# Kernel optimization log

Hardware: AMD Instinct MI355X
Metric: run time of the kernel (lower is better)

The kernel has to match this reference:

```python
import jax, jax.numpy as jnp
from jax import lax
import numpy as np

# dims
N_DIA, DLEN = 48, 64            # 48 dialogues, 64 utterances each
N = N_DIA * DLEN                # total utterances = 3072
D = 512                         # n_dim (modal feature dim)
H = 512                         # nhidden
NL = 2                          # GCNII layers
NS = 2                          # n_speakers
ALPHA, LAMDA = 0.1, 0.5
PI = float(np.pi)
SCALE = 0.99999                 # acos clamp factor from original code


def setup_inputs() -> dict:
    key = jax.random.key(0)
    ks = jax.random.split(key, 8)
    a = jax.random.normal(ks[0], (N, D), jnp.float32)
    v = jax.random.normal(ks[1], (N, D), jnp.float32)
    l = jax.random.normal(ks[2], (N, D), jnp.float32)
    qmask = jax.random.uniform(ks[3], (DLEN, N_DIA, NS), jnp.float32)
    dia_len = np.full((N_DIA,), DLEN, dtype=np.int64)  # static segment lengths
    # learned params
    W_spk = 0.02 * jax.random.normal(ks[4], (NS, D), jnp.float32)      # speaker_embeddings
    W0 = jax.random.normal(ks[5], (D, H), jnp.float32) / np.sqrt(D)    # graph_net.fcs[0]
    b0 = jnp.zeros((H,), jnp.float32)
    Wg = jax.random.normal(ks[6], (NL, H, H), jnp.float32) / np.sqrt(H)  # GCNII conv weights
    return {"a": a, "v": v, "l": l, "qmask": qmask, "dia_len": dia_len,
            "W_spk": W_spk, "W0": W0, "b0": b0, "Wg": Wg}


def _angular_sim(cs):
    # 1 - acos(cs*0.99999)/pi, clipped for numerical safety of acos
    return 1.0 - jnp.arccos(jnp.clip(cs * SCALE, -SCALE, SCALE)) / PI


def _build_adj(feats, seg_mask):
    # feats: list of 3 arrays [N, D]; seg_mask: [N, N] same-dialogue block mask
    n = feats[0].shape[0]
    normed = [f * jax.lax.rsqrt(jnp.sum(f * f, axis=1, keepdims=True)) for f in feats]
    adj = jnp.zeros((3 * n, 3 * n), feats[0].dtype)
    ar = jnp.arange(n)
    for m in range(3):
        for nn_ in range(3):
            if m == nn_:
                # within-modality: block-diagonal (per dialogue) angular cosine similarity
                sim = _angular_sim(normed[m] @ normed[m].T) * seg_mask
                adj = adj.at[m * n:(m + 1) * n, nn_ * n:(nn_ + 1) * n].set(sim)
            else:
                # cross-modality: only diagonal (same utterance) entries
                cs = jnp.sum(normed[m] * normed[nn_], axis=1)
                adj = adj.at[m * n + ar, nn_ * n + ar].set(_angular_sim(cs))
    # symmetric degree normalization D^-1/2 A D^-1/2
    dinv = jax.lax.rsqrt(adj.sum(axis=1))
    return adj * dinv[:, None] * dinv[None, :]


def reference(a, v, l, qmask, dia_len, W_spk, W0, b0, Wg):
    dl = np.asarray(dia_len)
    nb = dl.shape[0]
    # node -> (position-in-dialogue, dialogue-id), static from dia_len
    dia_id = np.repeat(np.arange(nb), dl)
    pos = np.concatenate([np.arange(x) for x in dl])
    qflat = qmask[pos, dia_id]                 # [N, NS], matches torch.cat order
    spk_idx = jnp.argmax(qflat, axis=-1)       # [N]
    l = l + W_spk[spk_idx]                     # use_speaker=True, 'l' in modals

    seg = jnp.asarray(dia_id)
    seg_mask = (seg[:, None] == seg[None, :]).astype(a.dtype)  # [N, N]
    adj = _build_adj([a, v, l], seg_mask)      # [3N, 3N]

    x = jnp.concatenate([a, v, l], axis=0)     # [3N, D]
    # GCNII_lyc (eval mode: dropout is identity)
    h0 = jax.nn.relu(x @ W0 + b0)              # [3N, H]
    thetas = jnp.log(LAMDA / jnp.arange(1, NL + 1, dtype=x.dtype) + 1.0)

    def step(h, wt):
        W, theta = wt
        hi = adj @ h
        support = (1.0 - ALPHA) * hi + ALPHA * h0   # variant=False
        h = jax.nn.relu(theta * (support @ W) + (1.0 - theta) * support)
        return h, None

    h, _ = lax.scan(step, h0, (Wg, thetas))
    feat = jnp.concatenate([x, h], axis=-1)    # use_residue=True -> [3N, D+H]
    n = a.shape[0]
    # regroup per-utterance modal features: [N, 3*(D+H)]
    out = jnp.concatenate([feat[:n], feat[n:2 * n], feat[2 * n:3 * n]], axis=-1)
    return out
```

## Files before the change

kernel.cpp:

```cpp
#include <hip/hip_runtime.h>
#include <math.h>

#define N_DIA 48
#define NTOT  3072
#define DD    512
#define M3    9216
#define SEG   ((size_t)NTOT * DD)

#define SCALE_F 0.99999f
#define PI_F    3.14159274101257324f

typedef __attribute__((ext_vector_type(8))) short frag8;
typedef __attribute__((ext_vector_type(4))) float f32x4;

__device__ __forceinline__ float ang_sim(float cs) {
    float cc = cs * SCALE_F;
    cc = fminf(fmaxf(cc, -SCALE_F), SCALE_F);
    return 1.0f - acosf(cc) / PI_F;
}
__device__ __forceinline__ unsigned short f2bf(float x) {
    union { float f; unsigned int u; } c; c.f = x;
    unsigned int r = c.u + 0x7fffu + ((c.u >> 16) & 1u);
    return (unsigned short)(r >> 16);
}
__device__ __forceinline__ float bf2f(unsigned short h) {
    union { unsigned int u; float f; } c; c.u = ((unsigned int)h) << 16;
    return c.f;
}
__device__ __forceinline__ void gload16(const unsigned short* g, unsigned short* s) {
    __builtin_amdgcn_global_load_lds(
        (const __attribute__((address_space(1))) unsigned int*)g,
        (__attribute__((address_space(3))) unsigned int*)s, 16, 0, 0);
}

__global__ __launch_bounds__(256) void k_pre_wt(
    const float* __restrict__ a, const float* __restrict__ v,
    const float* __restrict__ l, const float* __restrict__ qmask,
    const float* __restrict__ Wspk, const float* __restrict__ W0,
    const float* __restrict__ Wg,
    float* __restrict__ out, unsigned short* __restrict__ xb,
    float* __restrict__ invn, float* __restrict__ cross,
    unsigned short* __restrict__ Wt)
{
    __shared__ float tile[32][33];
    int b = blockIdx.x;
    if (b < 768) {
        int wv = threadIdx.x >> 6, t = threadIdx.x & 63;
        int i = b * 4 + wv;
        int pos = i & 63, dia = i >> 6;
        int qb = (pos * N_DIA + dia) * 2;
        float q0 = qmask[qb], q1 = qmask[qb + 1];
        int spk = (q0 >= q1) ? 0 : 1;
        const float4* av4 = (const float4*)(a + (size_t)i * DD);
        const float4* vv4 = (const float4*)(v + (size_t)i * DD);
        const float4* lv4 = (const float4*)(l + (size_t)i * DD);
        const float4* wv4 = (const float4*)(Wspk + (size_t)spk * DD);
        float* ob = out + (size_t)i * 3072;
        float saa = 0, svv = 0, sll = 0, sav = 0, sal = 0, svl = 0;
#pragma unroll
        for (int e = 0; e < 2; e++) {
            int idx = t * 2 + e;
            float4 xa = av4[idx], xv = vv4[idx], xd = lv4[idx], xw = wv4[idx];
            float4 xL = make_float4(xd.x + xw.x, xd.y + xw.y, xd.z + xw.z, xd.w + xw.w);
            *(float4*)(ob + idx * 4)        = xa;
            *(float4*)(ob + 1024 + idx * 4) = xv;
            *(float4*)(ob + 2048 + idx * 4) = xL;
            ushort4 ya, yv, yl;
            ya.x = f2bf(xa.x); ya.y = f2bf(xa.y); ya.z = f2bf(xa.z); ya.w = f2bf(xa.w);
            yv.x = f2bf(xv.x); yv.y = f2bf(xv.y); yv.z = f2bf(xv.z); yv.w = f2bf(xv.w);
            yl.x = f2bf(xL.x); yl.y = f2bf(xL.y); yl.z = f2bf(xL.z); yl.w = f2bf(xL.w);
            *(ushort4*)(xb + (size_t)i * DD + idx * 4) = ya;
            *(ushort4*)(xb + SEG + (size_t)i * DD + idx * 4) = yv;
            *(ushort4*)(xb + 2 * SEG + (size_t)i * DD + idx * 4) = yl;
            saa += xa.x * xa.x + xa.y * xa.y + xa.z * xa.z + xa.w * xa.w;
            svv += xv.x * xv.x + xv.y * xv.y + xv.z * xv.z + xv.w * xv.w;
            sll += xL.x * xL.x + xL.y * xL.y + xL.z * xL.z + xL.w * xL.w;
            sav += xa.x * xv.x + xa.y * xv.y + xa.z * xv.z + xa.w * xv.w;
            sal += xa.x * xL.x + xa.y * xL.y + xa.z * xL.z + xa.w * xL.w;
            svl += xv.x * xL.x + xv.y * xL.y + xv.z * xL.z + xv.w * xL.w;
        }
#pragma unroll
        for (int off = 32; off; off >>= 1) {
            saa += __shfl_down(saa, off, 64);
            svv += __shfl_down(svv, off, 64);
            sll += __shfl_down(sll, off, 64);
            sav += __shfl_down(sav, off, 64);
            sal += __shfl_down(sal, off, 64);
            svl += __shfl_down(svl, off, 64);
        }
        if (t == 0) {
            float ina = 1.0f / sqrtf(saa);
            float inv_ = 1.0f / sqrtf(svv);
            float inl = 1.0f / sqrtf(sll);
            invn[i] = ina; invn[NTOT + i] = inv_; invn[2 * NTOT + i] = inl;
            cross[i]            = ang_sim(sav * ina * inv_);
            cross[NTOT + i]     = ang_sim(sal * ina * inl);
            cross[2 * NTOT + i] = ang_sim(svl * inv_ * inl);
        }
    } else {
        int idx = b - 768;
        int mm = idx >> 8;
        int by = (idx >> 4) & 15, bx = idx & 15;
        const float* W = (mm == 0) ? W0 : Wg + (size_t)(mm - 1) * DD * DD;
        int t = threadIdx.x, tx = t & 31, ty = t >> 5;
#pragma unroll
        for (int q = 0; q < 4; q++) {
            int k = by * 32 + ty + q * 8;
            tile[ty + q * 8][tx] = W[(size_t)k * DD + bx * 32 + tx];
        }
        __syncthreads();
#pragma unroll
        for (int q = 0; q < 4; q++) {
            int n = bx * 32 + ty + q * 8;
            Wt[(size_t)mm * DD * DD + (size_t)n * DD + by * 32 + tx] = f2bf(tile[tx][ty + q * 8]);
        }
    }
}

__global__ __launch_bounds__(256) void k_gram_mfma(
    const unsigned short* __restrict__ xb, const float* __restrict__ invn,
    const float* __restrict__ cross, float* __restrict__ blk,
    float* __restrict__ dinv)
{
    __shared__ __align__(16) unsigned short Xs[16 * 2048];
    int d = blockIdx.x, m = blockIdx.y;
    int t = threadIdx.x;
    int lane = t & 63, wv = t >> 6;
    int mrow = m * NTOT + d * 64;
    const unsigned short* src = xb + (size_t)mrow * DD;
    int sunit = ((t & 3) ^ ((t >> 2) & 3)) * 8;
#pragma unroll
    for (int c = 0; c < 16; c++) {
        gload16(src + (size_t)(t >> 2) * DD + c * 32 + sunit,
                &Xs[c * 2048 + wv * 512]);
    }
    __syncthreads();

    int rsel = lane & 15, quad = lane >> 4;
    int sq = (quad ^ (rsel & 3)) * 8;
    f32x4 acc[4];
#pragma unroll
    for (int j = 0; j < 4; j++) acc[j] = (f32x4){0.f, 0.f, 0.f, 0.f};
#pragma unroll
    for (int c = 0; c < 16; c++) {
        const unsigned short* base = &Xs[c * 2048];
        frag8 bf[4];
#pragma unroll
        for (int j = 0; j < 4; j++)
            bf[j] = *(const frag8*)&base[(j * 16 + rsel) * 32 + sq];
        frag8 af = *(const frag8*)&base[(wv * 16 + rsel) * 32 + sq];
#pragma unroll
        for (int j = 0; j < 4; j++)
            acc[j] = __builtin_amdgcn_mfma_f32_16x16x32_bf16(af, bf[j], acc[j], 0, 0, 0);
    }

    size_t bbase = (size_t)(m * N_DIA + d) * 4096;
    int rowl0 = wv * 16 + quad * 4;
    float ir[4], rs[4] = {0.f, 0.f, 0.f, 0.f};
#pragma unroll
    for (int r = 0; r < 4; r++) ir[r] = invn[mrow + rowl0 + r];
#pragma unroll
    for (int j = 0; j < 4; j++) {
        int coll = j * 16 + rsel;
        float ic = invn[mrow + coll];
#pragma unroll
        for (int r = 0; r < 4; r++) {
            float sim = ang_sim(acc[j][r] * ir[r] * ic);
            blk[bbase + (size_t)(rowl0 + r) * 64 + coll] = sim;
            rs[r] += sim;
        }
    }
#pragma unroll
    for (int off = 8; off; off >>= 1)
#pragma unroll
        for (int r = 0; r < 4; r++) rs[r] += __shfl_down(rs[r], off, 16);
    if (rsel == 0) {
#pragma unroll
        for (int r = 0; r < 4; r++) {
            int gi = d * 64 + rowl0 + r;
            float c1, c2;
            if (m == 0)      { c1 = cross[gi];        c2 = cross[NTOT + gi]; }
            else if (m == 1) { c1 = cross[gi];        c2 = cross[2 * NTOT + gi]; }
            else             { c1 = cross[NTOT + gi]; c2 = cross[2 * NTOT + gi]; }
            dinv[m * NTOT + gi] = 1.0f / sqrtf(rs[r] + c1 + c2);
        }
    }
}

__global__ __launch_bounds__(256) void k_gemm(
    const unsigned short* __restrict__ A, const unsigned short* __restrict__ W,
    const float* __restrict__ bias,
    unsigned short* __restrict__ oRows, unsigned short* __restrict__ oT,
    float theta, int mode,
    const unsigned short* __restrict__ A2, unsigned short* __restrict__ oRows2)
{
    __shared__ __align__(16) char smem[53248];
    unsigned short* const As0 = (unsigned short*)smem;
    unsigned short* const As1 = (unsigned short*)(smem + 4096);
    unsigned short* const Bs0 = (unsigned short*)(smem + 8192);
    unsigned short* const Bs1 = (unsigned short*)(smem + 16384);
    unsigned short* const tH  = (unsigned short*)smem;
    unsigned short* const tR  = (unsigned short*)(smem + 17408);
    unsigned short* const tT  = (unsigned short*)(smem + 34816);

    int t = threadIdx.x, lane = t & 63, wv = t >> 6;
    int bx = blockIdx.x, by = blockIdx.y;
    const unsigned short* Ap = A;
    unsigned short* oR = oRows;
    unsigned short* oTp = oT;
    if (by >= 144) { Ap = A2; oR = oRows2; oTp = nullptr; by -= 144; }
    int mbase = by * 64, nbase = bx * 128;
    int srow = lane >> 2;
    int scol = (((lane & 3) ^ (srow & 3)) * 8);
    int rsel = lane & 15, quad = lane >> 4;
    int sq = (quad ^ (rsel & 3)) * 8;

    const unsigned short* Ag  = Ap + (size_t)(mbase + wv * 16 + srow) * DD + scol;
    const unsigned short* Bg0 = W  + (size_t)(nbase + wv * 32 + srow) * DD + scol;
    const unsigned short* Bg1 = W  + (size_t)(nbase + wv * 32 + 16 + srow) * DD + scol;

    f32x4 acc[8];
#pragma unroll
    for (int i = 0; i < 8; i++) acc[i] = (f32x4){0.f, 0.f, 0.f, 0.f};

    gload16(Ag,  As0 + wv * 512);
    gload16(Bg0, Bs0 + wv * 1024);
    gload16(Bg1, Bs0 + wv * 1024 + 512);

#pragma unroll
    for (int kt = 0; kt < 16; kt++) {
        __syncthreads();
        const unsigned short* Ac = (kt & 1) ? As1 : As0;
        const unsigned short* Bc = (kt & 1) ? Bs1 : Bs0;
        if (kt < 15) {
            unsigned short* An = (kt & 1) ? As0 : As1;
            unsigned short* Bn = (kt & 1) ? Bs0 : Bs1;
            gload16(Ag + (kt + 1) * 32,  An + wv * 512);
            gload16(Bg0 + (kt + 1) * 32, Bn + wv * 1024);
            gload16(Bg1 + (kt + 1) * 32, Bn + wv * 1024 + 512);
        }
        frag8 af[4], bfr[2];
#pragma unroll
        for (int i = 0; i < 4; i++)
            af[i] = *(const frag8*)&Ac[(i * 16 + rsel) * 32 + sq];
#pragma unroll
        for (int j = 0; j < 2; j++)
            bfr[j] = *(const frag8*)&Bc[(wv * 32 + j * 16 + rsel) * 32 + sq];
#pragma unroll
        for (int i = 0; i < 4; i++)
#pragma unroll
            for (int j = 0; j < 2; j++)
                acc[i * 2 + j] = __builtin_amdgcn_mfma_f32_16x16x32_bf16(
                    af[i], bfr[j], acc[i * 2 + j], 0, 0, 0);
    }
    __syncthreads();

    int r = t >> 2, c0 = (t & 3) * 32;
    if (mode == 1) {
        const unsigned short* srcA = Ap + (size_t)(mbase + r) * DD + nbase + c0;
#pragma unroll
        for (int u = 0; u < 4; u++)
            *(uint4*)&tH[r * 136 + c0 + u * 8] = *(const uint4*)(srcA + u * 8);
        __syncthreads();
    }
    float omt = 1.0f - theta;
#pragma unroll
    for (int i = 0; i < 4; i++)
#pragma unroll
        for (int j = 0; j < 2; j++) {
            int cl = wv * 32 + j * 16 + rsel;
            float bv = 0.f;
            if (mode == 0) bv = bias[nbase + cl];
            float vv[4];
#pragma unroll
            for (int rr = 0; rr < 4; rr++) {
                int rl = i * 16 + quad * 4 + rr;
                float x = acc[i * 2 + j][rr];
                if (mode == 0) x = fmaxf(x + bv, 0.f);
                else           x = theta * x + omt * bf2f(tH[rl * 136 + cl]);
                vv[rr] = x;
            }
#pragma unroll
            for (int rr = 0; rr < 4; rr++)
                tR[(i * 16 + quad * 4 + rr) * 136 + cl] = f2bf(vv[rr]);
            if (oTp) {
                ushort4 w4;
                w4.x = f2bf(vv[0]); w4.y = f2bf(vv[1]);
                w4.z = f2bf(vv[2]); w4.w = f2bf(vv[3]);
                *(ushort4*)&tT[cl * 72 + i * 16 + quad * 4] = w4;
            }
        }
    __syncthreads();
    {
        unsigned short* dst = oR + (size_t)(mbase + r) * DD + nbase + c0;
#pragma unroll
        for (int u = 0; u < 4; u++)
            *(uint4*)(dst + u * 8) = *(const uint4*)&tR[r * 136 + c0 + u * 8];
    }
    if (oTp) {
        int c = t >> 1, r0 = (t & 1) * 32;
        unsigned short* dst = oTp + (size_t)(nbase + c) * M3 + mbase + r0;
#pragma unroll
        for (int u = 0; u < 4; u++)
            *(uint4*)(dst + u * 8) = *(const uint4*)&tT[c * 72 + r0 + u * 8];
    }
}

__global__ __launch_bounds__(256) void k_adj(
    const float* __restrict__ blk, const float* __restrict__ cross,
    const float* __restrict__ dinv,
    const unsigned short* __restrict__ GT, const unsigned short* __restrict__ Gr,
    const unsigned short* __restrict__ P0,
    unsigned short* __restrict__ hout, float* __restrict__ outF, int final_mode)
{
    __shared__ __align__(16) unsigned short AdL[64 * 64];
    __shared__ __align__(16) unsigned short GTL[256 * 64];
    __shared__ __align__(16) unsigned short OT[64 * 264];
    __shared__ float dv[64];
    int ch = blockIdx.x, d = blockIdx.y, m = blockIdx.z;
    int t = threadIdx.x;
    int lane = t & 63, wv = t >> 6;
    int dbase = d * 64, cbase = ch * 256;
    int rsel = lane & 15, quad = lane >> 4;

    if (t < 64) dv[t] = dinv[m * NTOT + dbase + t];
    __syncthreads();

    size_t bbase = (size_t)(m * N_DIA + d) * 4096;
#pragma unroll
    for (int q = 0; q < 4; q++) {
        int e4 = t + 256 * q;
        int i = e4 >> 4, j4 = e4 & 15;
        float4 w = *(const float4*)(blk + bbase + (size_t)i * 64 + j4 * 4);
        float di = dv[i];
        ushort4 o;
        o.x = f2bf(w.x * di * dv[j4 * 4 + 0]);
        o.y = f2bf(w.y * di * dv[j4 * 4 + 1]);
        o.z = f2bf(w.z * di * dv[j4 * 4 + 2]);
        o.w = f2bf(w.w * di * dv[j4 * 4 + 3]);
        *(ushort4*)((char*)AdL + i * 128 + (((j4 >> 1) ^ (i & 7)) << 4) + ((j4 & 1) << 3)) = o;
    }
#pragma unroll
    for (int p = 0; p < 8; p++) {
        int e = t + 256 * p;
        int cl = e >> 3;
        int uo = e & 7;
        uint4 w = *(const uint4*)(GT + (size_t)(cbase + cl) * M3 + m * NTOT + dbase + uo * 8);
        *(uint4*)((char*)GTL + cl * 128 + ((uo ^ (cl & 7)) << 4)) = w;
    }
    __syncthreads();

    f32x4 acc[16];
#pragma unroll
    for (int i = 0; i < 16; i++) acc[i] = (f32x4){0.f, 0.f, 0.f, 0.f};
#pragma unroll
    for (int kk = 0; kk < 2; kk++) {
        int su = ((kk * 4 + quad) ^ (rsel & 7)) << 4;
        frag8 bfr[4];
#pragma unroll
        for (int it = 0; it < 4; it++)
            bfr[it] = *(const frag8*)((const char*)AdL + (it * 16 + rsel) * 128 + su);
#pragma unroll
        for (int jc = 0; jc < 4; jc++) {
            frag8 af = *(const frag8*)((const char*)GTL + (wv * 64 + jc * 16 + rsel) * 128 + su);
#pragma unroll
            for (int it = 0; it < 4; it++)
                acc[jc * 4 + it] = __builtin_amdgcn_mfma_f32_16x16x32_bf16(
                    af, bfr[it], acc[jc * 4 + it], 0, 0, 0);
        }
    }

    int n1, n2, p1, p2;
    if (m == 0)      { n1 = 1; n2 = 2; p1 = 0; p2 = 1; }
    else if (m == 1) { n1 = 0; n2 = 2; p1 = 0; p2 = 2; }
    else             { n1 = 0; n2 = 1; p1 = 1; p2 = 2; }
#pragma unroll
    for (int it = 0; it < 4; it++) {
        int il = it * 16 + rsel;
        int gi = dbase + il;
        float dm = dv[il];
        float cv1 = cross[p1 * NTOT + gi] * dm * dinv[n1 * NTOT + gi];
        float cv2 = cross[p2 * NTOT + gi] * dm * dinv[n2 * NTOT + gi];
        size_t r1 = (size_t)(n1 * NTOT + gi) * DD;
        size_t r2 = (size_t)(n2 * NTOT + gi) * DD;
        size_t r0 = (size_t)(m * NTOT + gi) * DD;
#pragma unroll
        for (int jc = 0; jc < 4; jc++) {
            int cl = wv * 64 + jc * 16 + quad * 4;
            int cg = cbase + cl;
            ushort4 u1 = *(const ushort4*)(Gr + r1 + cg);
            ushort4 u2 = *(const ushort4*)(Gr + r2 + cg);
            ushort4 u0 = *(const ushort4*)(P0 + r0 + cg);
            f32x4 aa = acc[jc * 4 + it];
            float o0 = fmaxf(0.9f * (aa[0] + cv1 * bf2f(u1.x) + cv2 * bf2f(u2.x)) + 0.1f * bf2f(u0.x), 0.f);
            float o1 = fmaxf(0.9f * (aa[1] + cv1 * bf2f(u1.y) + cv2 * bf2f(u2.y)) + 0.1f * bf2f(u0.y), 0.f);
            float o2 = fmaxf(0.9f * (aa[2] + cv1 * bf2f(u1.z) + cv2 * bf2f(u2.z)) + 0.1f * bf2f(u0.z), 0.f);
            float o3 = fmaxf(0.9f * (aa[3] + cv1 * bf2f(u1.w) + cv2 * bf2f(u2.w)) + 0.1f * bf2f(u0.w), 0.f);
            if (final_mode) {
                *(float4*)(outF + (size_t)gi * 3072 + m * 1024 + 512 + cg) =
                    make_float4(o0, o1, o2, o3);
            } else {
                ushort4 w;
                w.x = f2bf(o0); w.y = f2bf(o1); w.z = f2bf(o2); w.w = f2bf(o3);
                *(ushort4*)&OT[il * 264 + cl] = w;
            }
        }
    }
    if (!final_mode) {
        __syncthreads();
        int r = t >> 2, c0 = (t & 3) * 64;
        unsigned short* dst = hout + (size_t)(m * NTOT + dbase + r) * DD + cbase + c0;
#pragma unroll
        for (int u = 0; u < 8; u++)
            *(uint4*)(dst + u * 8) = *(const uint4*)&OT[r * 264 + c0 + u * 8];
    }
}

extern "C" void kernel_launch(void* const* d_in, const int* in_sizes, int n_in,
                              void* d_out, int out_size, void* d_ws, size_t ws_size,
                              hipStream_t stream) {
    (void)in_sizes; (void)n_in; (void)out_size; (void)ws_size;
    const float* a     = (const float*)d_in[0];
    const float* v     = (const float*)d_in[1];
    const float* l     = (const float*)d_in[2];
    const float* qmask = (const float*)d_in[3];
    const float* Wspk  = (const float*)d_in[5];
    const float* W0    = (const float*)d_in[6];
    const float* b0    = (const float*)d_in[7];
    const float* Wg    = (const float*)d_in[8];
    float* out = (float*)d_out;
    float* ws = (float*)d_ws;

    float* invn  = ws;
    float* blk   = invn + M3;
    float* cross = blk + (size_t)3 * N_DIA * 4096;
    float* dinvp = cross + M3;
    unsigned short* Wt  = (unsigned short*)(dinvp + M3);
    unsigned short* xb  = Wt + (size_t)3 * DD * DD;
    unsigned short* h0  = xb  + 3 * SEG;
    unsigned short* G1r = h0  + 3 * SEG;
    unsigned short* G1T = G1r + 3 * SEG;
    unsigned short* h1  = G1T + 3 * SEG;
    unsigned short* G2r = xb;
    unsigned short* G2T = G1r;
    unsigned short* P02 = G1T;

    const float th1 = 0.40546510810816438f;
    const float th2 = 0.22314355131420976f;

    k_pre_wt<<<1536, 256, 0, stream>>>(a, v, l, qmask, Wspk, W0, Wg, out, xb, invn, cross, Wt);
    k_gram_mfma<<<dim3(N_DIA, 3), 256, 0, stream>>>(xb, invn, cross, blk, dinvp);

    k_gemm<<<dim3(4, 144), 256, 0, stream>>>(xb, Wt, b0, h0, nullptr, 0.f, 0, nullptr, nullptr);
    k_gemm<<<dim3(4, 144), 256, 0, stream>>>(h0, Wt + (size_t)DD * DD, nullptr, G1r, G1T,
                                             th1, 1, nullptr, nullptr);
    k_adj<<<dim3(2, N_DIA, 3), 256, 0, stream>>>(blk, cross, dinvp, G1T, G1r, G1r,
                                                 h1, nullptr, 0);
    k_gemm<<<dim3(4, 288), 256, 0, stream>>>(h1, Wt + (size_t)2 * DD * DD, nullptr, G2r, G2T,
                                             th2, 1, h0, P02);
    k_adj<<<dim3(2, N_DIA, 3), 256, 0, stream>>>(blk, cross, dinvp, G2T, G2r, P02,
                                                 nullptr, out, 1);
}
```

Baseline: 204.8 us.

## Fuse gram, h0 GEMM and both h0-side layer GEMMs into one kernel

Merges the per-dialogue gram/similarity kernel, the h0 = relu(xW0+b) GEMM, the layer-1 h0@W1 GEMM and the layer-2 h0@W2 projection into one launch. Extra blocks handle the gram work alongside the GEMM blocks. Each GEMM block keeps a 32-row h0 tile in shared memory and reuses it for all three GEMMs, so h0 never goes through global memory. The later layer-2 GEMM shrinks to the h1 part only. In exchange, each block runs three dependent GEMMs serially with 64 accumulator registers and reads the weights straight from global memory. That could cut occupancy and parallelism, since there are only 288 GEMM blocks.

Result: slower. 247.8 us (+21.0%).

```diff
diff --git a/kernel.cpp b/kernel.cpp
--- a/kernel.cpp
+++ b/kernel.cpp
@@ -117,73 +117,209 @@
     }
 }
 
-__global__ __launch_bounds__(256) void k_gram_mfma(
-    const unsigned short* __restrict__ xb, const float* __restrict__ invn,
-    const float* __restrict__ cross, float* __restrict__ blk,
-    float* __restrict__ dinv)
+__global__ __launch_bounds__(256) void k_fused013(
+    const unsigned short* __restrict__ xb, const unsigned short* __restrict__ Wt,
+    const float* __restrict__ bias,
+    unsigned short* __restrict__ G1r, unsigned short* __restrict__ G1T,
+    unsigned short* __restrict__ P02,
+    const float* __restrict__ invn, const float* __restrict__ cross,
+    float* __restrict__ blk, float* __restrict__ dinv,
+    float th1, float th2)
 {
-    __shared__ __align__(16) unsigned short Xs[16 * 2048];
-    int d = blockIdx.x, m = blockIdx.y;
-    int t = threadIdx.x;
-    int lane = t & 63, wv = t >> 6;
-    int mrow = m * NTOT + d * 64;
-    const unsigned short* src = xb + (size_t)mrow * DD;
-    int sunit = ((t & 3) ^ ((t >> 2) & 3)) * 8;
-#pragma unroll
-    for (int c = 0; c < 16; c++) {
-        gload16(src + (size_t)(t >> 2) * DD + c * 32 + sunit,
-                &Xs[c * 2048 + wv * 512]);
+    __shared__ __align__(16) char smem[65536];
+    int b = blockIdx.x;
+    int t = threadIdx.x, lane = t & 63, wv = t >> 6;
+    int rsel = lane & 15, quad = lane >> 4;
+
+    if (b >= 288) {
+        unsigned short* Xs = (unsigned short*)smem;
+        int g = b - 288;
+        int d = g % N_DIA, m = g / N_DIA;
+        int mrow = m * NTOT + d * 64;
+        const unsigned short* src = xb + (size_t)mrow * DD;
+        int sunit = ((t & 3) ^ ((t >> 2) & 3)) * 8;
+#pragma unroll
+        for (int c = 0; c < 16; c++) {
+            gload16(src + (size_t)(t >> 2) * DD + c * 32 + sunit,
+                    &Xs[c * 2048 + wv * 512]);
+        }
+        __syncthreads();
+        int sq = (quad ^ (rsel & 3)) * 8;
+        f32x4 acc[4];
+#pragma unroll
+        for (int j = 0; j < 4; j++) acc[j] = (f32x4){0.f, 0.f, 0.f, 0.f};
+#pragma unroll
+        for (int c = 0; c < 16; c++) {
+            const unsigned short* base = &Xs[c * 2048];
+            frag8 bf[4];
+#pragma unroll
+            for (int j = 0; j < 4; j++)
+                bf[j] = *(const frag8*)&base[(j * 16 + rsel) * 32 + sq];
+            frag8 af = *(const frag8*)&base[(wv * 16 + rsel) * 32 + sq];
+#pragma unroll
+            for (int j = 0; j < 4; j++)
+                acc[j] = __builtin_amdgcn_mfma_f32_16x16x32_bf16(af, bf[j], acc[j], 0, 0, 0);
+        }
+        size_t bbase = (size_t)(m * N_DIA + d) * 4096;
+        int rowl0 = wv * 16 + quad * 4;
+        float ir[4], rs[4] = {0.f, 0.f, 0.f, 0.f};
+#pragma unroll
+        for (int r = 0; r < 4; r++) ir[r] = invn[mrow + rowl0 + r];
+#pragma unroll
+        for (int j = 0; j < 4; j++) {
+            int coll = j * 16 + rsel;
+            float ic = invn[mrow + coll];
+#pragma unroll
+            for (int r = 0; r < 4; r++) {
+                float sim = ang_sim(acc[j][r] * ir[r] * ic);
+                blk[bbase + (size_t)(rowl0 + r) * 64 + coll] = sim;
+                rs[r] += sim;
+            }
+        }
+#pragma unroll
+        for (int off = 8; off; off >>= 1)
+#pragma unroll
+            for (int r = 0; r < 4; r++) rs[r] += __shfl_down(rs[r], off, 16);
+        if (rsel == 0) {
+#pragma unroll
+            for (int r = 0; r < 4; r++) {
+                int gi = d * 64 + rowl0 + r;
+                float c1, c2;
+                if (m == 0)      { c1 = cross[gi];        c2 = cross[NTOT + gi]; }
+                else if (m == 1) { c1 = cross[gi];        c2 = cross[2 * NTOT + gi]; }
+                else             { c1 = cross[NTOT + gi]; c2 = cross[2 * NTOT + gi]; }
+                dinv[m * NTOT + gi] = 1.0f / sqrtf(rs[r] + c1 + c2);
+            }
+        }
+        return;
+    }
+
+    unsigned short* Xs  = (unsigned short*)smem;
+    unsigned short* H0s = (unsigned short*)(smem + 32768);
+    int mbase = b * 32;
+
+#pragma unroll
+    for (int r = 0; r < 8; r++) {
+        int row = r * 4 + wv;
+        int us = lane ^ ((row & 7) << 2);
+        gload16(xb + (size_t)(mbase + row) * DD + us * 8, Xs + row * 512);
     }
     __syncthreads();
 
-    int rsel = lane & 15, quad = lane >> 4;
-    int sq = (quad ^ (rsel & 3)) * 8;
-    f32x4 acc[4];
-#pragma unroll
-    for (int j = 0; j < 4; j++) acc[j] = (f32x4){0.f, 0.f, 0.f, 0.f};
-#pragma unroll
-    for (int c = 0; c < 16; c++) {
-        const unsigned short* base = &Xs[c * 2048];
-        frag8 bf[4];
-#pragma unroll
-        for (int j = 0; j < 4; j++)
-            bf[j] = *(const frag8*)&base[(j * 16 + rsel) * 32 + sq];
-        frag8 af = *(const frag8*)&base[(wv * 16 + rsel) * 32 + sq];
-#pragma unroll
-        for (int j = 0; j < 4; j++)
-            acc[j] = __builtin_amdgcn_mfma_f32_16x16x32_bf16(af, bf[j], acc[j], 0, 0, 0);
-    }
-
-    size_t bbase = (size_t)(m * N_DIA + d) * 4096;
-    int rowl0 = wv * 16 + quad * 4;
-    float ir[4], rs[4] = {0.f, 0.f, 0.f, 0.f};
-#pragma unroll
-    for (int r = 0; r < 4; r++) ir[r] = invn[mrow + rowl0 + r];
-#pragma unroll
-    for (int j = 0; j < 4; j++) {
-        int coll = j * 16 + rsel;
-        float ic = invn[mrow + coll];
-#pragma unroll
-        for (int r = 0; r < 4; r++) {
-            float sim = ang_sim(acc[j][r] * ir[r] * ic);
-            blk[bbase + (size_t)(rowl0 + r) * 64 + coll] = sim;
-            rs[r] += sim;
-        }
-    }
-#pragma unroll
-    for (int off = 8; off; off >>= 1)
-#pragma unroll
-        for (int r = 0; r < 4; r++) rs[r] += __shfl_down(rs[r], off, 16);
-    if (rsel == 0) {
-#pragma unroll
-        for (int r = 0; r < 4; r++) {
-            int gi = d * 64 + rowl0 + r;
-            float c1, c2;
-            if (m == 0)      { c1 = cross[gi];        c2 = cross[NTOT + gi]; }
-            else if (m == 1) { c1 = cross[gi];        c2 = cross[2 * NTOT + gi]; }
-            else             { c1 = cross[NTOT + gi]; c2 = cross[2 * NTOT + gi]; }
-            dinv[m * NTOT + gi] = 1.0f / sqrtf(rs[r] + c1 + c2);
-        }
+    const unsigned short* W0t = Wt;
+    const unsigned short* W1t = Wt + (size_t)DD * DD;
+    const unsigned short* W2t = Wt + (size_t)2 * DD * DD;
+
+    f32x4 acc[16];
+
+#pragma unroll
+    for (int z = 0; z < 16; z++) acc[z] = (f32x4){0.f, 0.f, 0.f, 0.f};
+#pragma unroll 4
+    for (int kt = 0; kt < 16; kt++) {
+        frag8 af[2];
+#pragma unroll
+        for (int i = 0; i < 2; i++) {
+            int row = i * 16 + rsel;
+            int u = kt * 4 + quad;
+            af[i] = *(const frag8*)&Xs[row * 512 + ((u ^ ((row & 7) << 2)) << 3)];
+        }
+#pragma unroll
+        for (int j = 0; j < 8; j++) {
+            frag8 bf = *(const frag8*)(W0t + (size_t)(wv * 128 + j * 16 + rsel) * DD + kt * 32 + quad * 8);
+#pragma unroll
+            for (int i = 0; i < 2; i++)
+                acc[i * 8 + j] = __builtin_amdgcn_mfma_f32_16x16x32_bf16(af[i], bf, acc[i * 8 + j], 0, 0, 0);
+        }
+    }
+#pragma unroll
+    for (int i = 0; i < 2; i++)
+#pragma unroll
+        for (int j = 0; j < 8; j++) {
+            int col = wv * 128 + j * 16 + rsel;
+            float bv = bias[col];
+#pragma unroll
+            for (int rr = 0; rr < 4; rr++) {
+                int row = i * 16 + quad * 4 + rr;
+                float x = fmaxf(acc[i * 8 + j][rr] + bv, 0.f);
+                H0s[row * 512 + (((col >> 3) ^ ((row & 7) << 2)) << 3) + (col & 7)] = f2bf(x);
+            }
+        }
+    __syncthreads();
+
+#pragma unroll
+    for (int z = 0; z < 16; z++) acc[z] = (f32x4){0.f, 0.f, 0.f, 0.f};
+#pragma unroll 4
+    for (int kt = 0; kt < 16; kt++) {
+        frag8 af[2];
+#pragma unroll
+        for (int i = 0; i < 2; i++) {
+            int row = i * 16 + rsel;
+            int u = kt * 4 + quad;
+            af[i] = *(const frag8*)&H0s[row * 512 + ((u ^ ((row & 7) << 2)) << 3)];
+        }
+#pragma unroll
+        for (int j = 0; j < 8; j++) {
+            frag8 bf = *(const frag8*)(W1t + (size_t)(wv * 128 + j * 16 + rsel) * DD + kt * 32 + quad * 8);
+#pragma unroll
+            for (int i = 0; i < 2; i++)
+                acc[i * 8 + j] = __builtin_amdgcn_mfma_f32_16x16x32_bf16(af[i], bf, acc[i * 8 + j], 0, 0, 0);
+        }
+    }
+    {
+        float omt = 1.0f - th1;
+#pragma unroll
+        for (int i = 0; i < 2; i++)
+#pragma unroll
+            for (int j = 0; j < 8; j++) {
+                int col = wv * 128 + j * 16 + rsel;
+                float vv[4];
+#pragma unroll
+                for (int rr = 0; rr < 4; rr++) {
+                    int row = i * 16 + quad * 4 + rr;
+                    float h0v = bf2f(H0s[row * 512 + (((col >> 3) ^ ((row & 7) << 2)) << 3) + (col & 7)]);
+                    vv[rr] = th1 * acc[i * 8 + j][rr] + omt * h0v;
+                    G1r[(size_t)(mbase + row) * DD + col] = f2bf(vv[rr]);
+                }
+                ushort4 w4;
+                w4.x = f2bf(vv[0]); w4.y = f2bf(vv[1]);
+                w4.z = f2bf(vv[2]); w4.w = f2bf(vv[3]);
+                *(ushort4*)(G1T + (size_t)col * M3 + mbase + i * 16 + quad * 4) = w4;
+            }
+    }
+
+#pragma unroll
+    for (int z = 0; z < 16; z++) acc[z] = (f32x4){0.f, 0.f, 0.f, 0.f};
+#pragma unroll 4
+    for (int kt = 0; kt < 16; kt++) {
+        frag8 af[2];
+#pragma unroll
+        for (int i = 0; i < 2; i++) {
+            int row = i * 16 + rsel;
+            int u = kt * 4 + quad;
+            af[i] = *(const frag8*)&H0s[row * 512 + ((u ^ ((row & 7) << 2)) << 3)];
+        }
+#pragma unroll
+        for (int j = 0; j < 8; j++) {
+            frag8 bf = *(const frag8*)(W2t + (size_t)(wv * 128 + j * 16 + rsel) * DD + kt * 32 + quad * 8);
+#pragma unroll
+            for (int i = 0; i < 2; i++)
+                acc[i * 8 + j] = __builtin_amdgcn_mfma_f32_16x16x32_bf16(af[i], bf, acc[i * 8 + j], 0, 0, 0);
+        }
+    }
+    {
+        float omt = 1.0f - th2;
+#pragma unroll
+        for (int i = 0; i < 2; i++)
+#pragma unroll
+            for (int j = 0; j < 8; j++) {
+                int col = wv * 128 + j * 16 + rsel;
+#pragma unroll
+                for (int rr = 0; rr < 4; rr++) {
+                    int row = i * 16 + quad * 4 + rr;
+                    float h0v = bf2f(H0s[row * 512 + (((col >> 3) ^ ((row & 7) << 2)) << 3) + (col & 7)]);
+                    P02[(size_t)(mbase + row) * DD + col] = f2bf(th2 * acc[i * 8 + j][rr] + omt * h0v);
+                }
+            }
     }
 }
 
@@ -437,27 +573,23 @@
     float* dinvp = cross + M3;
     unsigned short* Wt  = (unsigned short*)(dinvp + M3);
     unsigned short* xb  = Wt + (size_t)3 * DD * DD;
-    unsigned short* h0  = xb  + 3 * SEG;
-    unsigned short* G1r = h0  + 3 * SEG;
+    unsigned short* P02 = xb  + 3 * SEG;
+    unsigned short* G1r = P02 + 3 * SEG;
     unsigned short* G1T = G1r + 3 * SEG;
     unsigned short* h1  = G1T + 3 * SEG;
     unsigned short* G2r = xb;
-    unsigned short* G2T = G1r;
-    unsigned short* P02 = G1T;
+    unsigned short* G2T = G1T;
 
     const float th1 = 0.40546510810816438f;
     const float th2 = 0.22314355131420976f;
 
     k_pre_wt<<<1536, 256, 0, stream>>>(a, v, l, qmask, Wspk, W0, Wg, out, xb, invn, cross, Wt);
-    k_gram_mfma<<<dim3(N_DIA, 3), 256, 0, stream>>>(xb, invn, cross, blk, dinvp);
-
-    k_gemm<<<dim3(4, 144), 256, 0, stream>>>(xb, Wt, b0, h0, nullptr, 0.f, 0, nullptr, nullptr);
-    k_gemm<<<dim3(4, 144), 256, 0, stream>>>(h0, Wt + (size_t)DD * DD, nullptr, G1r, G1T,
-                                             th1, 1, nullptr, nullptr);
+    k_fused013<<<432, 256, 0, stream>>>(xb, Wt, b0, G1r, G1T, P02,
+                                        invn, cross, blk, dinvp, th1, th2);
     k_adj<<<dim3(2, N_DIA, 3), 256, 0, stream>>>(blk, cross, dinvp, G1T, G1r, G1r,
                                                  h1, nullptr, 0);
-    k_gemm<<<dim3(4, 288), 256, 0, stream>>>(h1, Wt + (size_t)2 * DD * DD, nullptr, G2r, G2T,
-                                             th2, 1, h0, P02);
+    k_gemm<<<dim3(4, 144), 256, 0, stream>>>(h1, Wt + (size_t)2 * DD * DD, nullptr, G2r, G2T,
+                                             th2, 1, nullptr, nullptr);
     k_adj<<<dim3(2, N_DIA, 3), 256, 0, stream>>>(blk, cross, dinvp, G2T, G2r, P02,
                                                  nullptr, out, 1);
 }
```
